# Optimization experiments

Hardware: AMD Instinct MI355X
Metric: run time of the kernel (lower is better)

## Reference

```python
import jax, jax.numpy as jnp
import numpy as np

B, N, D = 4, 4096, 1024
HEADS = 4
DH = D // HEADS
FF = 4 * D
EPS = 1e-5


def layer_norm(x, g, b):
    mu = jnp.mean(x, axis=-1, keepdims=True)
    var = jnp.mean(jnp.square(x - mu), axis=-1, keepdims=True)
    return (x - mu) * jax.lax.rsqrt(var + EPS) * g + b


def linear_attn(q, k, v):
    # q,k,v: [b, h, n, dh]; non-causal kernelized linear attention
    scale = DH ** -0.25
    q = jax.nn.softmax(q * scale, axis=-1)   # feature map over head dim
    k = jax.nn.softmax(k * scale, axis=-2)   # normalized over sequence
    context = jnp.einsum('bhnd,bhne->bhde', k, v)  # [b,h,dh,dh]
    return jnp.einsum('bhnd,bhde->bhne', q, context)


def setup_inputs() -> dict:
    key = jax.random.key(0)
    ks = jax.random.split(key, 16)
    s = lambda fan_in: 1.0 / np.sqrt(fan_in)
    inp = {
        'x': jax.random.normal(ks[0], (B, N, D), jnp.float32),
        # attention block (PreNorm)
        'ln1_g': jnp.ones((D,), jnp.float32),
        'ln1_b': jnp.zeros((D,), jnp.float32),
        'wq': jax.random.normal(ks[1], (D, D), jnp.float32) * s(D),
        'wk': jax.random.normal(ks[2], (D, D), jnp.float32) * s(D),
        'wv': jax.random.normal(ks[3], (D, D), jnp.float32) * s(D),
        'wo': jax.random.normal(ks[4], (D, D), jnp.float32) * s(D),
        'bo': jnp.zeros((D,), jnp.float32),
        # feedforward block (PreNorm)
        'ln2_g': jnp.ones((D,), jnp.float32),
        'ln2_b': jnp.zeros((D,), jnp.float32),
        'w_ff1': jax.random.normal(ks[5], (D, FF), jnp.float32) * s(D),
        'b_ff1': jnp.zeros((FF,), jnp.float32),
        'w_ff2': jax.random.normal(ks[6], (FF, D), jnp.float32) * s(FF),
        'b_ff2': jnp.zeros((D,), jnp.float32),
        # trailing dense
        'w_d': jax.random.normal(ks[7], (D, D), jnp.float32) * s(D),
        'b_d': jnp.zeros((D,), jnp.float32),
    }
    return inp


def reference(x, ln1_g, ln1_b, wq, wk, wv, wo, bo, ln2_g, ln2_b,
              w_ff1, b_ff1, w_ff2, b_ff2, w_d, b_d):
    b, n, d = x.shape
    # --- PreNorm linear self-attention + residual ---
    h = layer_norm(x, ln1_g, ln1_b)
    q = (h @ wq).reshape(b, n, HEADS, DH).transpose(0, 2, 1, 3)
    k = (h @ wk).reshape(b, n, HEADS, DH).transpose(0, 2, 1, 3)
    v = (h @ wv).reshape(b, n, HEADS, DH).transpose(0, 2, 1, 3)
    attn = linear_attn(q, k, v)                      # [b,h,n,dh]
    attn = attn.transpose(0, 2, 1, 3).reshape(b, n, d)
    x = x + attn @ wo + bo
    # --- PreNorm FFN (GELU, mult=4) + residual ---
    h = layer_norm(x, ln2_g, ln2_b)
    x = x + jax.nn.gelu(h @ w_ff1 + b_ff1) @ w_ff2 + b_ff2
    # --- trailing dense projection ---
    return x @ w_d + b_d
```

## Files before the change

### kernel.cpp

```cpp
#include <hip/hip_runtime.h>
#include <hip/hip_bf16.h>


typedef __hip_bfloat16 bf16;
typedef __attribute__((ext_vector_type(8))) short short8;
typedef __attribute__((ext_vector_type(4))) float floatx4;

__device__ __forceinline__ float b2f(bf16 x) { return __bfloat162float(x); }
__device__ __forceinline__ bf16 f2b(float x) { return __float2bfloat16(x); }
__device__ __forceinline__ float s2f(short s) {
  unsigned int u = ((unsigned int)(unsigned short)s) << 16;
  return __uint_as_float(u);
}
__device__ __forceinline__ short f2s(float f) {
  bf16 h = __float2bfloat16(f);
  return *reinterpret_cast<short*>(&h);
}
__device__ __forceinline__ float gelu_f(float x) {
  float u = 0.7978845608028654f * (x + 0.044715f * x * x * x);
  return 0.5f * x * (1.0f + tanhf(u));
}

template <int TRANSC, int AFP32, int CFP32, int ATOM, int RESF32 = 0>
__global__ __launch_bounds__(256) void gemm_bt(
    const void* __restrict__ Aop, const bf16* __restrict__ BT, void* Cv,
    int K, int lda, int ldb, int ldc, int zshift,
    long saA, long shA, long saB, long shB, long saC, long shC,
    const float* __restrict__ bias, const bf16* res, int act,
    const float2* stats, const float* __restrict__ gamma,
    const float* __restrict__ beta)
{
  int z = blockIdx.z;
  int zb = z >> zshift, zh = z & ((1 << zshift) - 1);
  long offA = (long)zb * saA + (long)zh * shA;
  long offC = (long)zb * saC + (long)zh * shC;
  const float* Af = (const float*)Aop + offA;
  const bf16*  Ab = (const bf16*)Aop + offA;
  BT += (long)zb * saB + (long)zh * shB;
  bf16*  C  = (bf16*)Cv + offC;
  float* Cf = (float*)Cv + offC;
  const bf16*  resb = res ? res + offC : nullptr;
  const float* resf = res ? (const float*)res + offC : nullptr;
  if (stats) stats += offA / lda;

  __shared__ bf16 smem[TRANSC ? 128 * 136 : 16384];
  bf16* As = smem;
  bf16* Bs = smem + 8192;

  const int t = threadIdx.x;
  const int w = t >> 6, l = t & 63;
  const int m0 = blockIdx.y * 128, n0 = blockIdx.x * 128;
  const int wm = (w >> 1) * 64, wn = (w & 1) * 64;
  const int lr = l & 15, lq = l >> 4;

  floatx4 acc[4][4] = {};

  const int sr = t >> 2;
  const int sc = (t & 3) * 8;
  const int stO = sr * 32 + (((t & 3) ^ ((sr >> 1) & 3))) * 8;
  const int rowA0 = m0 + sr, rowA1 = m0 + 64 + sr;
  const long o0 = (long)rowA0 * lda + sc;
  const long o1 = (long)rowA1 * lda + sc;

  const bf16* Bp0 = BT + (long)(n0 + sr) * ldb + sc;
  const bf16* Bp1 = BT + (long)(n0 + 64 + sr) * ldb + sc;

  float2 st0, st1;
  if (stats) { st0 = stats[rowA0]; st1 = stats[rowA1]; }

  auto LOADSET = [&](int k0, short8& ra0, short8& ra1, short8& rb0, short8& rb1) {
    if constexpr (AFP32) {
      float4 a00 = *(const float4*)(Af + o0 + k0);
      float4 a01 = *(const float4*)(Af + o0 + k0 + 4);
      float4 a10 = *(const float4*)(Af + o1 + k0);
      float4 a11 = *(const float4*)(Af + o1 + k0 + 4);
      float v0[8] = {a00.x, a00.y, a00.z, a00.w, a01.x, a01.y, a01.z, a01.w};
      float v1[8] = {a10.x, a10.y, a10.z, a10.w, a11.x, a11.y, a11.z, a11.w};
      if (stats) {
        float4 g0 = *(const float4*)(gamma + k0 + sc);
        float4 g1 = *(const float4*)(gamma + k0 + sc + 4);
        float4 e0 = *(const float4*)(beta + k0 + sc);
        float4 e1 = *(const float4*)(beta + k0 + sc + 4);
        float gv[8] = {g0.x, g0.y, g0.z, g0.w, g1.x, g1.y, g1.z, g1.w};
        float ev[8] = {e0.x, e0.y, e0.z, e0.w, e1.x, e1.y, e1.z, e1.w};
#pragma unroll
        for (int i = 0; i < 8; i++) {
          v0[i] = (v0[i] - st0.x) * st0.y * gv[i] + ev[i];
          v1[i] = (v1[i] - st1.x) * st1.y * gv[i] + ev[i];
        }
      }
#pragma unroll
      for (int i = 0; i < 8; i++) { ra0[i] = f2s(v0[i]); ra1[i] = f2s(v1[i]); }
    } else {
      ra0 = *(const short8*)(Ab + o0 + k0);
      ra1 = *(const short8*)(Ab + o1 + k0);
      if (stats) {
        float4 g0 = *(const float4*)(gamma + k0 + sc);
        float4 g1 = *(const float4*)(gamma + k0 + sc + 4);
        float4 e0 = *(const float4*)(beta + k0 + sc);
        float4 e1 = *(const float4*)(beta + k0 + sc + 4);
        float gv[8] = {g0.x, g0.y, g0.z, g0.w, g1.x, g1.y, g1.z, g1.w};
        float ev[8] = {e0.x, e0.y, e0.z, e0.w, e1.x, e1.y, e1.z, e1.w};
#pragma unroll
        for (int i = 0; i < 8; i++) {
          ra0[i] = f2s((s2f(ra0[i]) - st0.x) * st0.y * gv[i] + ev[i]);
          ra1[i] = f2s((s2f(ra1[i]) - st1.x) * st1.y * gv[i] + ev[i]);
        }
      }
    }
    short8 b0 = *(const short8*)(Bp0 + k0);
    short8 b1 = *(const short8*)(Bp1 + k0);
    rb0 = b0; rb1 = b1;
  };

  auto STORESET = [&](int p, short8 ra0, short8 ra1, short8 rb0, short8 rb1) {
    *(short8*)&As[p * 4096 + stO]        = ra0;
    *(short8*)&As[p * 4096 + 2048 + stO] = ra1;
    *(short8*)&Bs[p * 4096 + stO]        = rb0;
    *(short8*)&Bs[p * 4096 + 2048 + stO] = rb1;
  };

  auto COMPUTE = [&](int p) {
    short8 af[4], bfr[4];
#pragma unroll
    for (int i = 0; i < 4; i++) {
      int Ra = wm + i * 16 + lr;
      int Rb = wn + i * 16 + lr;
      af[i]  = *(const short8*)&As[p * 4096 + Ra * 32 + (lq ^ ((Ra >> 1) & 3)) * 8];
      bfr[i] = *(const short8*)&Bs[p * 4096 + Rb * 32 + (lq ^ ((Rb >> 1) & 3)) * 8];
    }
#pragma unroll
    for (int i = 0; i < 4; i++)
#pragma unroll
      for (int j = 0; j < 4; j++)
        acc[i][j] = __builtin_amdgcn_mfma_f32_16x16x32_bf16(af[i], bfr[j], acc[i][j], 0, 0, 0);
  };

  short8 pa0, pa1, pb0, pb1, qa0, qa1, qb0, qb1;
  LOADSET(0,  pa0, pa1, pb0, pb1);
  LOADSET(32, qa0, qa1, qb0, qb1);
  STORESET(0, pa0, pa1, pb0, pb1);
  __syncthreads();
  const int nI = K >> 5;
  for (int it = 0; it < nI; it += 2) {
    if (it + 2 < nI) LOADSET((it + 2) * 32, pa0, pa1, pb0, pb1);
    COMPUTE(0);
    STORESET(1, qa0, qa1, qb0, qb1);
    __syncthreads();
    if (it + 3 < nI) LOADSET((it + 3) * 32, qa0, qa1, qb0, qb1);
    COMPUTE(1);
    if (it + 2 < nI) STORESET(0, pa0, pa1, pb0, pb1);
    __syncthreads();
  }

  if constexpr (TRANSC) {
    bf16* TC = smem;
#pragma unroll
    for (int i = 0; i < 4; i++) {
      int rloc = wm + i * 16 + lq * 4;
#pragma unroll
      for (int j = 0; j < 4; j++) {
        int cloc = wn + j * 16 + lr;
#pragma unroll
        for (int r = 0; r < 4; r++)
          TC[cloc * 136 + rloc + r] = f2b(acc[i][j][r]);
      }
    }
    __syncthreads();
    long base = (long)n0 * ldc + m0;
#pragma unroll
    for (int p = 0; p < 8; p++) {
      int er = (t >> 4) + p * 16;
      int mc = (t & 15) * 8;
      *(short8*)(C + base + (long)er * ldc + mc) = *(const short8*)&TC[er * 136 + mc];
    }
    return;
  }

#pragma unroll
  for (int i = 0; i < 4; i++) {
    int row0 = m0 + wm + i * 16 + lq * 4;
#pragma unroll
    for (int j = 0; j < 4; j++) {
      int col = n0 + wn + j * 16 + lr;
      if constexpr (ATOM) {
#pragma unroll
        for (int r = 0; r < 4; r++) {
          long idx = (long)(row0 + r) * ldc + col;
          atomicAdd(&Cf[idx], acc[i][j][r]);
        }
      } else {
        float bv = bias ? bias[col] : 0.0f;
#pragma unroll
        for (int r = 0; r < 4; r++) {
          float v = acc[i][j][r] + bv;
          long idx = (long)(row0 + r) * ldc + col;
          if (res) {
            if constexpr (RESF32) v += resf[idx]; else v += b2f(resb[idx]);
          }
          if (act) v = gelu_f(v);
          if constexpr (CFP32) Cf[idx] = v; else C[idx] = f2b(v);
        }
      }
    }
  }
}

__global__ void transpose_f2b(const float* __restrict__ src, bf16* __restrict__ dst,
                              int lsrc, int ldst)
{
  __shared__ bf16 tile[32][33];
  int tx = threadIdx.x, ty = threadIdx.y;
  int c0 = blockIdx.x * 32, r0 = blockIdx.y * 32;
#pragma unroll
  for (int j = 0; j < 4; j++)
    tile[ty + j * 8][tx] = f2b(src[(long)(r0 + ty + j * 8) * lsrc + c0 + tx]);
  __syncthreads();
#pragma unroll
  for (int j = 0; j < 4; j++)
    dst[(long)(c0 + ty + j * 8) * ldst + r0 + tx] = tile[tx][ty + j * 8];
}

__global__ __launch_bounds__(128) void copy_cols(const bf16* __restrict__ s,
                                                 bf16* __restrict__ d)
{
  int r = blockIdx.x, c = threadIdx.x * 8;
  *(short8*)(d + (long)r * 5120 + 4096 + c) = *(const short8*)(s + (long)r * 1024 + c);
}

__global__ __launch_bounds__(256) void ln_stats_f32(
    const float* __restrict__ x, float2* __restrict__ stats)
{
  int row = blockIdx.x, t = threadIdx.x;
  const float* xr = x + (long)row * 1024;
  float4 a = *(const float4*)(xr + t * 4);
  float s = a.x + a.y + a.z + a.w;
  float q = a.x * a.x + a.y * a.y + a.z * a.z + a.w * a.w;
  for (int o = 32; o > 0; o >>= 1) { s += __shfl_down(s, o); q += __shfl_down(q, o); }
  __shared__ float sm[8];
  if ((t & 63) == 0) { sm[t >> 6] = s; sm[4 + (t >> 6)] = q; }
  __syncthreads();
  if (t == 0) {
    s = sm[0] + sm[1] + sm[2] + sm[3];
    q = sm[4] + sm[5] + sm[6] + sm[7];
    float mean = s * (1.0f / 1024.0f);
    float var  = q * (1.0f / 1024.0f) - mean * mean;
    stats[row] = make_float2(mean, rsqrtf(var + 1e-5f));
  }
}

__global__ __launch_bounds__(256) void ln_apply(
    const float* __restrict__ x, const float2* __restrict__ stats,
    const float* __restrict__ g, const float* __restrict__ b,
    bf16* __restrict__ out)
{
  long i = ((long)blockIdx.x * 256 + threadIdx.x) * 8;
  int row = (int)(i >> 10), col = (int)(i & 1023);
  float2 st = stats[row];
  float4 a0 = *(const float4*)(x + i);
  float4 a1 = *(const float4*)(x + i + 4);
  float4 g0 = *(const float4*)(g + col);
  float4 g1 = *(const float4*)(g + col + 4);
  float4 b0 = *(const float4*)(b + col);
  float4 b1 = *(const float4*)(b + col + 4);
  float av[8] = {a0.x, a0.y, a0.z, a0.w, a1.x, a1.y, a1.z, a1.w};
  float gv[8] = {g0.x, g0.y, g0.z, g0.w, g1.x, g1.y, g1.z, g1.w};
  float bv[8] = {b0.x, b0.y, b0.z, b0.w, b1.x, b1.y, b1.z, b1.w};
  short8 o;
#pragma unroll
  for (int j = 0; j < 8; j++)
    o[j] = f2s((av[j] - st.x) * st.y * gv[j] + bv[j]);
  *(short8*)(out + i) = o;
}

__global__ __launch_bounds__(256) void ln_stats_b16(
    const bf16* __restrict__ x, float2* __restrict__ stats)
{
  int row = blockIdx.x, t = threadIdx.x;
  const bf16* xr = x + (long)row * 1024;
  float v[4];
#pragma unroll
  for (int i = 0; i < 4; i++) v[i] = b2f(xr[t * 4 + i]);
  float s = v[0] + v[1] + v[2] + v[3];
  float q = v[0] * v[0] + v[1] * v[1] + v[2] * v[2] + v[3] * v[3];
  for (int o = 32; o > 0; o >>= 1) { s += __shfl_down(s, o); q += __shfl_down(q, o); }
  __shared__ float sm[8];
  if ((t & 63) == 0) { sm[t >> 6] = s; sm[4 + (t >> 6)] = q; }
  __syncthreads();
  if (t == 0) {
    s = sm[0] + sm[1] + sm[2] + sm[3];
    q = sm[4] + sm[5] + sm[6] + sm[7];
    float mean = s * (1.0f / 1024.0f);
    float var  = q * (1.0f / 1024.0f) - mean * mean;
    stats[row] = make_float2(mean, rsqrtf(var + 1e-5f));
  }
}

__global__ __launch_bounds__(256) void qsoftmax256(bf16* __restrict__ q)
{
  long idx = (long)blockIdx.x * 256 + threadIdx.x;
  int t = threadIdx.x;
  float v = expf(0.25f * b2f(q[idx]));
  float s = v;
  for (int o = 32; o > 0; o >>= 1) s += __shfl_down(s, o);
  __shared__ float sm[4];
  if ((t & 63) == 0) sm[t >> 6] = s;
  __syncthreads();
  float tot = sm[0] + sm[1] + sm[2] + sm[3];
  q[idx] = f2b(v / tot);
}

__global__ __launch_bounds__(256) void ksoftmaxKV(bf16* __restrict__ kv)
{
  int b = blockIdx.x >> 8, e = blockIdx.x & 255;
  long base = ((long)b * 512 + e) * 4096;
  int t = threadIdx.x;
  float loc[16];
  float s = 0.0f;
#pragma unroll
  for (int i = 0; i < 16; i++) {
    loc[i] = expf(0.25f * b2f(kv[base + t + i * 256]));
    s += loc[i];
  }
  for (int o = 32; o > 0; o >>= 1) s += __shfl_down(s, o);
  __shared__ float sm[4];
  if ((t & 63) == 0) sm[t >> 6] = s;
  __syncthreads();
  float inv = 1.0f / (sm[0] + sm[1] + sm[2] + sm[3]);
#pragma unroll
  for (int i = 0; i < 16; i++)
    kv[base + t + i * 256] = f2b(loc[i] * inv);
}

__global__ __launch_bounds__(256) void reduce_ctx(
    const bf16* __restrict__ G, bf16* __restrict__ dst)
{
  long i = (long)blockIdx.x * 256 + threadIdx.x;
  float s = 0.0f;
#pragma unroll
  for (int kc = 0; kc < 16; kc++) s += b2f(G[kc * 262144 + i]);
  dst[(i >> 16) * 262144 + (i & 65535)] = f2b(s);
}

__global__ __launch_bounds__(256) void out_bias(
    const float* __restrict__ b2, const bf16* __restrict__ wdt, int ld,
    const float* __restrict__ bd, float* __restrict__ OB)
{
  int n = blockIdx.x, t = threadIdx.x;
  const bf16* wr = wdt + (long)n * ld;
  float s = 0.0f;
#pragma unroll
  for (int i = 0; i < 4; i++) {
    int k = t * 4 + i;
    s += b2[k] * b2f(wr[k]);
  }
  for (int o = 32; o > 0; o >>= 1) s += __shfl_down(s, o);
  __shared__ float sm[4];
  if ((t & 63) == 0) sm[t >> 6] = s;
  __syncthreads();
  if (t == 0) OB[n] = sm[0] + sm[1] + sm[2] + sm[3] + bd[n];
}

__global__ __launch_bounds__(256) void bias_bcast(
    const float* __restrict__ b, float* __restrict__ out)
{
  long i = ((long)blockIdx.x * 256 + threadIdx.x) * 4;
  *(float4*)(out + i) = *(const float4*)(b + (int)(i & 1023));
}

extern "C" void kernel_launch(void* const* d_in, const int* in_sizes, int n_in,
                              void* d_out, int out_size, void* d_ws, size_t ws_size,
                              hipStream_t stream) {
  const float* x    = (const float*)d_in[0];
  const float* ln1g = (const float*)d_in[1];
  const float* ln1b = (const float*)d_in[2];
  const float* wq   = (const float*)d_in[3];
  const float* wk   = (const float*)d_in[4];
  const float* wv   = (const float*)d_in[5];
  const float* wo   = (const float*)d_in[6];
  const float* bo   = (const float*)d_in[7];
  const float* ln2g = (const float*)d_in[8];
  const float* ln2b = (const float*)d_in[9];
  const float* wff1 = (const float*)d_in[10];
  const float* bff1 = (const float*)d_in[11];
  const float* wff2 = (const float*)d_in[12];
  const float* bff2 = (const float*)d_in[13];
  const float* wd   = (const float*)d_in[14];
  const float* bd   = (const float*)d_in[15];

  bf16* xln = (bf16*)d_out;
  bf16* x2  = (bf16*)d_out + (size_t)16384 * 1024;
  float* outf = (float*)d_out;

  char* wsp = (char*)d_ws;
  size_t off = 0;
  auto alloc = [&](size_t bytes) -> void* {
    void* p = wsp + off; off += (bytes + 255) & ~(size_t)255; return p;
  };
  bf16*   S1  = (bf16*)alloc((size_t)8 * 1024 * 1024);
  bf16*   S2  = (bf16*)alloc((size_t)10 * 1024 * 1024);
  bf16*   G   = (bf16*)alloc((size_t)10 * 1024 * 1024);
  bf16*   CTX = (bf16*)alloc((size_t)4 * 256 * 256 * 2);
  bf16*   W1  = (bf16*)alloc((size_t)1024 * 256 * 2);
  float2* st1 = (float2*)alloc((size_t)16384 * 8);
  float2* st2 = (float2*)alloc((size_t)16384 * 8);
  bf16*   KV   = S1;
  bf16*   W1kv = G + (size_t)9 * 512 * 1024;
  bf16*   CTXT = S2 + (size_t)4 * 1024 * 1024;
  bf16*   woT  = G + (size_t)4 * 1024 * 1024;
  bf16*   CWT  = G;
  bf16*   wqT  = CTXT;
  bf16*   QB   = S1;
  bf16*   WB   = S2;
  float*  OB   = (float*)CTX;

  const long SA  = (long)4096 * 1024;
  const long PKV = (long)512 * 4096;
  dim3 tb(32, 8);
  const bf16* nb = nullptr;

  ln_stats_f32<<<16384, 256, 0, stream>>>(x, st1);
  ln_apply<<<8192, 256, 0, stream>>>(x, st1, ln1g, ln1b, xln);

  for (int h = 0; h < 4; h++) {
    transpose_f2b<<<dim3(8, 32), tb, 0, stream>>>(wk + h * 256, W1kv, 1024, 1024);
    transpose_f2b<<<dim3(8, 32), tb, 0, stream>>>(wv + h * 256, W1kv + 256 * 1024, 1024, 1024);
    gemm_bt<1, 0, 0, 0><<<dim3(4, 32, 4), 256, 0, stream>>>(xln, W1kv, KV,
        1024, 1024, 1024, 4096, 2, 0, SA, 0, 0, 0, PKV,
        nullptr, nb, 0, nullptr, nullptr, nullptr);
    ksoftmaxKV<<<1024, 256, 0, stream>>>(KV);

    gemm_bt<0, 0, 0, 0><<<dim3(2, 2, 64), 256, 0, stream>>>(KV, KV + (long)256 * 4096, G,
        256, 4096, 4096, 256, 4, PKV, 256, PKV, 256, 65536, 262144,
        nullptr, nb, 0, nullptr, nullptr, nullptr);
    reduce_ctx<<<1024, 256, 0, stream>>>(G, CTXT + h * 65536);
  }

  transpose_f2b<<<dim3(32, 32), tb, 0, stream>>>(wo, woT, 1024, 1024);
  gemm_bt<0, 0, 0, 0><<<dim3(2, 8, 16), 256, 0, stream>>>(woT, CTXT, CWT,
      256, 1024, 256, 1024, 2, 0, 256, 262144, 65536, 1048576, 256,
      nullptr, nb, 0, nullptr, nullptr, nullptr);
  transpose_f2b<<<dim3(32, 32), tb, 0, stream>>>(wq, wqT, 1024, 1024);

  for (int p = 0; p < 2; p++) {
    gemm_bt<0, 0, 0, 0><<<dim3(8, 64, 1), 256, 0, stream>>>(
        xln + (size_t)p * 8192 * 1024, wqT, QB,
        1024, 1024, 1024, 1024, 0, 0, 0, 0, 0, 0, 0,
        nullptr, nb, 0, nullptr, nullptr, nullptr);
    qsoftmax256<<<32768, 256, 0, stream>>>(QB);
    gemm_bt<0, 0, 0, 0, 1><<<dim3(8, 32, 2), 256, 0, stream>>>(
        QB, CWT + (size_t)p * 2 * 1048576, x2 + (size_t)p * 8192 * 1024,
        1024, 1024, 1024, 1024, 1, 0, SA, 0, 1048576, 0, SA,
        bo, (const bf16*)(x + (size_t)p * 8192 * 1024), 0,
        nullptr, nullptr, nullptr);
  }

  ln_stats_b16<<<16384, 256, 0, stream>>>(x2, st2);
  transpose_f2b<<<dim3(128, 32), tb, 0, stream>>>(wff1, S1, 4096, 1024);
  transpose_f2b<<<dim3(32, 32), tb, 0, stream>>>(wd, WB + 4096, 1024, 5120);
  gemm_bt<1, 1, 0, 0><<<dim3(8, 32, 1), 256, 0, stream>>>(wff2, WB + 4096, WB,
      1024, 1024, 5120, 5120, 0, 0, 0, 0, 0, 0, 0,
      nullptr, nb, 0, nullptr, nullptr, nullptr);
  out_bias<<<1024, 256, 0, stream>>>(bff2, WB + 4096, 5120, bd, OB);

  for (int R = 0; R < 16; R++) {
    const bf16* xr = x2 + (size_t)R * 1024 * 1024;
    copy_cols<<<1024, 128, 0, stream>>>(xr, G);
    gemm_bt<0, 0, 0, 0><<<dim3(32, 8, 1), 256, 0, stream>>>(xr, S1, G,
        1024, 1024, 1024, 5120, 2, 0, 0, 0, 0, 0, 0,
        bff1, nb, 1, st2 + R * 1024, ln2g, ln2b);
    bias_bcast<<<1024, 256, 0, stream>>>(OB, outf + (size_t)R * 1024 * 1024);
    gemm_bt<0, 0, 1, 1><<<dim3(8, 8, 4), 256, 0, stream>>>(G, WB,
        outf + (size_t)R * 1024 * 1024,
        1280, 5120, 5120, 1024, 2, 0, 1280, 0, 1280, 0, 0,
        nullptr, nb, 0, nullptr, nullptr, nullptr);
  }
}
```

Baseline: 1.970 ms.

## Remap GEMM workgroups across XCDs and fuse FFN prep copies

The GEMM kernel now remaps its linear workgroup id so that consecutive tiles are spread round-robin across the eight XCDs. The aim is better per-XCD L2 reuse of shared A/B panels on MI355X. The FFN loop fuses the column copy and the output bias broadcast into one ffn_prep kernel. It also reads the FF1 GEMM's A operand from the copied columns in G instead of from x2, which cuts launch count. The remap adds integer divisions per block and changes the tile traversal order, which could hurt locality for some grid shapes.

```diff
diff --git a/kernel.cpp b/kernel.cpp
--- a/kernel.cpp
+++ b/kernel.cpp
@@ -30,7 +30,16 @@
     const float2* stats, const float* __restrict__ gamma,
     const float* __restrict__ beta)
 {
-  int z = blockIdx.z;
+  unsigned gx = gridDim.x, gy = gridDim.y;
+  unsigned nxy = gx * gy, nwg = nxy * gridDim.z;
+  unsigned orig = blockIdx.y + gy * (blockIdx.x + gx * blockIdx.z);
+  unsigned sid = ((nwg & 7u) == 0u) ? ((orig & 7u) * (nwg >> 3) + (orig >> 3))
+                                    : orig;
+  unsigned bz = sid / nxy;
+  unsigned rr = sid - bz * nxy;
+  unsigned bxi = rr / gy, byi = rr - (rr / gy) * gy;
+
+  int z = (int)bz;
   int zb = z >> zshift, zh = z & ((1 << zshift) - 1);
   long offA = (long)zb * saA + (long)zh * shA;
   long offC = (long)zb * saC + (long)zh * shC;
@@ -49,7 +58,7 @@
 
   const int t = threadIdx.x;
   const int w = t >> 6, l = t & 63;
-  const int m0 = blockIdx.y * 128, n0 = blockIdx.x * 128;
+  const int m0 = (int)byi * 128, n0 = (int)bxi * 128;
   const int wm = (w >> 1) * 64, wn = (w & 1) * 64;
   const int lr = l & 15, lq = l >> 4;
 
@@ -219,6 +228,17 @@
 #pragma unroll
   for (int j = 0; j < 4; j++)
     dst[(long)(c0 + ty + j * 8) * ldst + r0 + tx] = tile[tx][ty + j * 8];
+}
+
+__global__ __launch_bounds__(256) void ffn_prep(
+    const bf16* __restrict__ x2c, const float* __restrict__ OB,
+    bf16* __restrict__ G, float* __restrict__ out)
+{
+  int r = blockIdx.x, t = threadIdx.x;
+  if (t < 128)
+    *(short8*)(G + (long)r * 5120 + 4096 + t * 8) =
+        *(const short8*)(x2c + (long)r * 1024 + t * 8);
+  *(float4*)(out + (long)r * 1024 + t * 4) = *(const float4*)(OB + t * 4);
 }
 
 __global__ __launch_bounds__(128) void copy_cols(const bf16* __restrict__ s,
@@ -465,13 +485,17 @@
 
   for (int R = 0; R < 16; R++) {
     const bf16* xr = x2 + (size_t)R * 1024 * 1024;
-    copy_cols<<<1024, 128, 0, stream>>>(xr, G);
-    gemm_bt<0, 0, 0, 0><<<dim3(32, 8, 1), 256, 0, stream>>>(xr, S1, G,
-        1024, 1024, 1024, 5120, 2, 0, 0, 0, 0, 0, 0,
+    float* outR = outf + (size_t)R * 1024 * 1024;
+    if (R < 15) {
+      ffn_prep<<<1024, 256, 0, stream>>>(xr, OB, G, outR);
+    } else {
+      copy_cols<<<1024, 128, 0, stream>>>(xr, G);
+      bias_bcast<<<1024, 256, 0, stream>>>(OB, outR);
+    }
+    gemm_bt<0, 0, 0, 0><<<dim3(32, 8, 1), 256, 0, stream>>>(G + 4096, S1, G,
+        1024, 5120, 1024, 5120, 2, 0, 0, 0, 0, 0, 0,
         bff1, nb, 1, st2 + R * 1024, ln2g, ln2b);
-    bias_bcast<<<1024, 256, 0, stream>>>(OB, outf + (size_t)R * 1024 * 1024);
-    gemm_bt<0, 0, 1, 1><<<dim3(8, 8, 4), 256, 0, stream>>>(G, WB,
-        outf + (size_t)R * 1024 * 1024,
+    gemm_bt<0, 0, 1, 1><<<dim3(8, 8, 4), 256, 0, stream>>>(G, WB, outR,
         1280, 5120, 5120, 1024, 2, 0, 1280, 0, 1280, 0, 0,
         nullptr, nb, 0, nullptr, nullptr, nullptr);
   }
```

Result: no change. 1.995 ms (+1.3%).
